# Optimization experiments

Measured on AMD Instinct MI355X. Metric: run time of the kernel, lower is better.

The kernel has to match this reference:

```python
import jax, jax.numpy as jnp
import numpy as np


def _dwconv(x, w, b, pad):
    # x: [B, C, H, W]; w: [C, 1, kh, kw]; depthwise via feature_group_count=C
    y = jax.lax.conv_general_dilated(
        x, w, window_strides=(1, 1), padding=pad,
        dimension_numbers=("NCHW", "OIHW", "NCHW"),
        feature_group_count=x.shape[1])
    return y + b[None, :, None, None]


def setup_inputs() -> dict:
    key = jax.random.key(0)
    ks = jax.random.split(key, 16)
    dim, B, H, W = 128, 32, 64, 64
    def w_init(k, shape):
        fan_in = int(np.prod(shape[1:]))
        return jax.random.normal(k, shape, jnp.float32) * (1.0 / np.sqrt(fan_in))
    return {
        "x": jax.random.normal(ks[0], (B, dim, H, W), jnp.float32),
        "w0": w_init(ks[1], (dim, 1, 5, 5)),   "b0": jax.random.normal(ks[2], (dim,), jnp.float32) * 0.01,
        "w0_1": w_init(ks[3], (dim, 1, 1, 7)), "b0_1": jax.random.normal(ks[4], (dim,), jnp.float32) * 0.01,
        "w0_2": w_init(ks[5], (dim, 1, 7, 1)), "b0_2": jax.random.normal(ks[6], (dim,), jnp.float32) * 0.01,
        "w1_1": w_init(ks[7], (dim, 1, 1, 15)), "b1_1": jax.random.normal(ks[8], (dim,), jnp.float32) * 0.01,
        "w1_2": w_init(ks[9], (dim, 1, 15, 1)), "b1_2": jax.random.normal(ks[10], (dim,), jnp.float32) * 0.01,
        "w2_1": w_init(ks[11], (dim, 1, 1, 31)), "b2_1": jax.random.normal(ks[12], (dim,), jnp.float32) * 0.01,
        "w2_2": w_init(ks[13], (dim, 1, 31, 1)), "b2_2": jax.random.normal(ks[14], (dim,), jnp.float32) * 0.01,
    }


def reference(x, w0, b0, w0_1, b0_1, w0_2, b0_2, w1_1, b1_1, w1_2, b1_2, w2_1, b2_1, w2_2, b2_2):
    attn = _dwconv(x, w0, b0, ((2, 2), (2, 2)))
    attn_0 = _dwconv(attn, w0_1, b0_1, ((0, 0), (3, 3)))
    attn_0 = _dwconv(attn_0, w0_2, b0_2, ((3, 3), (0, 0)))
    attn_1 = _dwconv(attn, w1_1, b1_1, ((0, 0), (7, 7)))
    attn_1 = _dwconv(attn_1, w1_2, b1_2, ((7, 7), (0, 0)))
    attn_2 = _dwconv(attn, w2_1, b2_1, ((0, 0), (15, 15)))
    attn_2 = _dwconv(attn_2, w2_2, b2_2, ((15, 15), (0, 0)))
    return jnp.concatenate((x, attn, attn_0, attn_1, attn_2), axis=1)
```

## Files before the change

kernel.cpp:

```cpp
#include <hip/hip_runtime.h>

#define TPB 256

#define XS_STRIDE 76
#define XS_SIZE   (68 * 76)

#define TS_STRIDE 68
#define TS_SIZE   (64 * 68)

__global__ __launch_bounds__(TPB, 4)
void lka_conv5_kernel(const float* __restrict__ x,
                      const float* __restrict__ w0, const float* __restrict__ b0,
                      float* __restrict__ out) {
    __shared__ __align__(16) float xs[XS_SIZE];
    const int tid = threadIdx.x;
    const int plane = blockIdx.x;
    const int b = plane >> 7;
    const int c = plane & 127;
    const float* xp = x + (size_t)plane * 4096;
    float* outb = out + ((size_t)b * 640 + (size_t)c) * 4096;

    {
        const float4 z4 = make_float4(0.f, 0.f, 0.f, 0.f);
        float4* u4 = (float4*)xs;
#pragma unroll
        for (int k = tid; k < XS_SIZE / 4; k += TPB) u4[k] = z4;
    }
    __syncthreads();
    {
        const float4* x4 = (const float4*)xp;
        float4* o4 = (float4*)outb;
#pragma unroll
        for (int s = 0; s < 4; ++s) {
            const int idx = tid + s * TPB;
            const float4 v = x4[idx];
            o4[idx] = v;
            const int r = idx >> 4;
            const int c0 = (idx & 15) << 2;
            *(float4*)&xs[(r + 2) * XS_STRIDE + c0 + 4] = v;
        }
    }
    __syncthreads();
    {
        const int i = tid >> 2;
        const int j0 = (tid & 3) << 4;
        const float* wp = w0 + c * 25;
        const float bias = b0[c];
        float acc[16];
#pragma unroll
        for (int jj = 0; jj < 16; ++jj) acc[jj] = bias;
#pragma unroll
        for (int a = 0; a < 5; ++a) {
            float raw[24];
#pragma unroll
            for (int k = 0; k < 6; ++k)
                *(float4*)&raw[4 * k] = *(const float4*)&xs[(i + a) * XS_STRIDE + j0 + 4 * k];
#pragma unroll
            for (int bb = 0; bb < 5; ++bb) {
                const float w = wp[a * 5 + bb];
#pragma unroll
                for (int jj = 0; jj < 16; ++jj) acc[jj] += raw[jj + bb + 2] * w;
            }
        }
        float* op = outb + (size_t)128 * 4096 + i * 64 + j0;
#pragma unroll
        for (int q = 0; q < 4; ++q)
            ((float4*)op)[q] = make_float4(acc[4 * q], acc[4 * q + 1],
                                           acc[4 * q + 2], acc[4 * q + 3]);
    }
}

template <int K>
__device__ __forceinline__ void branch_pass(
    const int tid, const int c,
    const float* __restrict__ att,
    const float* __restrict__ wh, const float* __restrict__ bh,
    const float* __restrict__ wv, const float* __restrict__ bv,
    float* __restrict__ op0, float* __restrict__ t) {
    constexpr int T = 2 * K + 1;
    constexpr int KA = K + 1;
    constexpr int NW4 = (KA + 16 + K + 3) / 4;
    constexpr int W = 16 + 2 * K;

    {
        const int i = tid >> 2;
        const int j0 = (tid & 3) << 4;
        const float* arow = att + i * 64;
        float raw[4 * NW4];
#pragma unroll
        for (int q = 0; q < NW4; ++q) {
            const int col0 = j0 - KA + 4 * q;
            const bool ok = (unsigned)col0 < 61u;
            const float4 v = *(const float4*)&arow[ok ? col0 : 0];
            raw[4 * q + 0] = ok ? v.x : 0.f;
            raw[4 * q + 1] = ok ? v.y : 0.f;
            raw[4 * q + 2] = ok ? v.z : 0.f;
            raw[4 * q + 3] = ok ? v.w : 0.f;
        }
        const float* whp = wh + c * T;
        const float bias = bh[c];
        float acc[16];
#pragma unroll
        for (int jj = 0; jj < 16; ++jj) acc[jj] = bias;
#pragma unroll
        for (int d = 0; d < T; ++d) {
            const float w = whp[d];
#pragma unroll
            for (int jj = 0; jj < 16; ++jj) acc[jj] += raw[jj + d + 1] * w;
        }
#pragma unroll
        for (int q = 0; q < 4; ++q)
            *(float4*)&t[i * TS_STRIDE + j0 + 4 * q] =
                make_float4(acc[4 * q], acc[4 * q + 1], acc[4 * q + 2], acc[4 * q + 3]);
    }
    __syncthreads();

    {
        const int j = tid & 63;
        const int i0 = (tid >> 6) << 4;
        float win[W];
#pragma unroll
        for (int dd = 0; dd < W; ++dd) {
            const int r = i0 - K + dd;
            const int rc = min(max(r, 0), 63);
            const float v = t[rc * TS_STRIDE + j];
            win[dd] = (r == rc) ? v : 0.f;
        }
        const float* wvp = wv + c * T;
        const float bias = bv[c];
        float acc[16];
#pragma unroll
        for (int ii = 0; ii < 16; ++ii) acc[ii] = bias;
#pragma unroll
        for (int d = 0; d < T; ++d) {
            const float w = wvp[d];
#pragma unroll
            for (int ii = 0; ii < 16; ++ii) acc[ii] += win[ii + d] * w;
        }
        float* op = op0 + i0 * 64 + j;
#pragma unroll
        for (int ii = 0; ii < 16; ++ii) op[ii * 64] = acc[ii];
    }
}

__global__ __launch_bounds__(TPB, 4)
void lka_branch_kernel(float* out,
                       const float* __restrict__ w01, const float* __restrict__ b01,
                       const float* __restrict__ w02, const float* __restrict__ b02,
                       const float* __restrict__ w11, const float* __restrict__ b11,
                       const float* __restrict__ w12, const float* __restrict__ b12,
                       const float* __restrict__ w21, const float* __restrict__ b21,
                       const float* __restrict__ w22, const float* __restrict__ b22) {
    __shared__ __align__(16) float t[TS_SIZE];
    const int tid = threadIdx.x;
    const int plane = blockIdx.x;
    const int b = plane >> 7;
    const int c = plane & 127;
    const float* att = out + ((size_t)b * 640 + 128 + (size_t)c) * 4096;
    float* op = out + ((size_t)b * 640 + (size_t)(2 + blockIdx.y) * 128 + (size_t)c) * 4096;

    if (blockIdx.y == 0)
        branch_pass<3>(tid, c, att, w01, b01, w02, b02, op, t);
    else if (blockIdx.y == 1)
        branch_pass<7>(tid, c, att, w11, b11, w12, b12, op, t);
    else
        branch_pass<15>(tid, c, att, w21, b21, w22, b22, op, t);
}

extern "C" void kernel_launch(void* const* d_in, const int* in_sizes, int n_in,
                              void* d_out, int out_size, void* d_ws, size_t ws_size,
                              hipStream_t stream) {
    const float* x   = (const float*)d_in[0];
    const float* w0  = (const float*)d_in[1];
    const float* b0  = (const float*)d_in[2];
    const float* w01 = (const float*)d_in[3];
    const float* b01 = (const float*)d_in[4];
    const float* w02 = (const float*)d_in[5];
    const float* b02 = (const float*)d_in[6];
    const float* w11 = (const float*)d_in[7];
    const float* b11 = (const float*)d_in[8];
    const float* w12 = (const float*)d_in[9];
    const float* b12 = (const float*)d_in[10];
    const float* w21 = (const float*)d_in[11];
    const float* b21 = (const float*)d_in[12];
    const float* w22 = (const float*)d_in[13];
    const float* b22 = (const float*)d_in[14];
    float* out = (float*)d_out;

    lka_conv5_kernel<<<dim3(4096), dim3(TPB), 0, stream>>>(x, w0, b0, out);
    lka_branch_kernel<<<dim3(4096, 3), dim3(TPB), 0, stream>>>(
        out, w01, b01, w02, b02, w11, b11, w12, b12, w21, b21, w22, b22);
}
```

Baseline: 450.4 us.

## Fuse 5x5 conv and all three separable branches into one per-plane kernel

Merges the two kernels into one block per (batch, channel) plane. The 5x5 depthwise result stays in LDS and feeds all three horizontal/vertical branch passes, so the attn plane is no longer re-read from global memory three times and one launch disappears. The zero-filled padded LDS tile is replaced by clamped, predicated loads, and __syncthreads is swapped for a raw lgkmcnt wait plus s_barrier. In exchange, each block runs the three branches serially with only 4096 blocks instead of 12288 and uses twice the LDS, which may lower occupancy and parallelism.

```diff
diff --git a/kernel.cpp b/kernel.cpp
--- a/kernel.cpp
+++ b/kernel.cpp
@@ -1,32 +1,110 @@
 #include <hip/hip_runtime.h>
 
 #define TPB 256
-
-#define XS_STRIDE 76
-#define XS_SIZE   (68 * 76)
 
 #define TS_STRIDE 68
 #define TS_SIZE   (64 * 68)
 
+__device__ __forceinline__ void sync_lds() {
+    asm volatile("s_waitcnt lgkmcnt(0)" ::: "memory");
+    __builtin_amdgcn_s_barrier();
+}
+
+template <int K>
+__device__ __forceinline__ void h_pass(const int tid, const int c,
+                                       const float* __restrict__ att,
+                                       const float* __restrict__ wh,
+                                       const float* __restrict__ bh,
+                                       float* __restrict__ t) {
+    constexpr int T = 2 * K + 1;
+    constexpr int KA = K + 1;
+    constexpr int NW4 = (KA + 16 + K + 3) / 4;
+    const int i = tid >> 2;
+    const int j0 = (tid & 3) << 4;
+    const float* wp = wh + c * T;
+    const float bias = bh[c];
+    const float* arow = att + i * TS_STRIDE;
+    float raw[4 * NW4];
+#pragma unroll
+    for (int q = 0; q < NW4; ++q) {
+        const int col0 = j0 - KA + 4 * q;
+        const bool ok = (unsigned)col0 < 61u;
+        const float4 v = *(const float4*)&arow[ok ? col0 : 0];
+        raw[4 * q + 0] = ok ? v.x : 0.f;
+        raw[4 * q + 1] = ok ? v.y : 0.f;
+        raw[4 * q + 2] = ok ? v.z : 0.f;
+        raw[4 * q + 3] = ok ? v.w : 0.f;
+    }
+    float acc[16];
+#pragma unroll
+    for (int jj = 0; jj < 16; ++jj) acc[jj] = bias;
+#pragma unroll
+    for (int d = 0; d < T; ++d) {
+        const float w = wp[d];
+#pragma unroll
+        for (int jj = 0; jj < 16; ++jj) acc[jj] += raw[jj + d + 1] * w;
+    }
+#pragma unroll
+    for (int q = 0; q < 4; ++q)
+        *(float4*)&t[i * TS_STRIDE + j0 + 4 * q] =
+            make_float4(acc[4 * q], acc[4 * q + 1], acc[4 * q + 2], acc[4 * q + 3]);
+}
+
+template <int K>
+__device__ __forceinline__ void v_pass(const int tid, const int c,
+                                       const float* __restrict__ t,
+                                       const float* __restrict__ wv,
+                                       const float* __restrict__ bv,
+                                       float* __restrict__ op0) {
+    constexpr int T = 2 * K + 1;
+    constexpr int W = 16 + 2 * K;
+    const int j = tid & 63;
+    const int i0 = (tid >> 6) << 4;
+    const float* wp = wv + c * T;
+    const float bias = bv[c];
+    float win[W];
+#pragma unroll
+    for (int dd = 0; dd < W; ++dd) {
+        const int r = i0 - K + dd;
+        const int rc = min(max(r, 0), 63);
+        const float v = t[rc * TS_STRIDE + j];
+        win[dd] = (r == rc) ? v : 0.f;
+    }
+    float acc[16];
+#pragma unroll
+    for (int ii = 0; ii < 16; ++ii) acc[ii] = bias;
+#pragma unroll
+    for (int d = 0; d < T; ++d) {
+        const float w = wp[d];
+#pragma unroll
+        for (int ii = 0; ii < 16; ++ii) acc[ii] += win[ii + d] * w;
+    }
+    float* op = op0 + i0 * 64 + j;
+#pragma unroll
+    for (int ii = 0; ii < 16; ++ii) op[ii * 64] = acc[ii];
+}
+
 __global__ __launch_bounds__(TPB, 4)
-void lka_conv5_kernel(const float* __restrict__ x,
-                      const float* __restrict__ w0, const float* __restrict__ b0,
+void lka_fused_kernel(const float* __restrict__ x,
+                      const float* __restrict__ w0,  const float* __restrict__ b0,
+                      const float* __restrict__ w01, const float* __restrict__ b01,
+                      const float* __restrict__ w02, const float* __restrict__ b02,
+                      const float* __restrict__ w11, const float* __restrict__ b11,
+                      const float* __restrict__ w12, const float* __restrict__ b12,
+                      const float* __restrict__ w21, const float* __restrict__ b21,
+                      const float* __restrict__ w22, const float* __restrict__ b22,
                       float* __restrict__ out) {
-    __shared__ __align__(16) float xs[XS_SIZE];
+    __shared__ __align__(16) float bufA[TS_SIZE];
+    __shared__ __align__(16) float bufB[TS_SIZE];
+
     const int tid = threadIdx.x;
     const int plane = blockIdx.x;
     const int b = plane >> 7;
     const int c = plane & 127;
+
     const float* xp = x + (size_t)plane * 4096;
     float* outb = out + ((size_t)b * 640 + (size_t)c) * 4096;
 
-    {
-        const float4 z4 = make_float4(0.f, 0.f, 0.f, 0.f);
-        float4* u4 = (float4*)xs;
-#pragma unroll
-        for (int k = tid; k < XS_SIZE / 4; k += TPB) u4[k] = z4;
-    }
-    __syncthreads();
     {
         const float4* x4 = (const float4*)xp;
         float4* o4 = (float4*)outb;
@@ -37,10 +115,11 @@
             o4[idx] = v;
             const int r = idx >> 4;
             const int c0 = (idx & 15) << 2;
-            *(float4*)&xs[(r + 2) * XS_STRIDE + c0 + 4] = v;
+            *(float4*)&bufA[r * TS_STRIDE + c0] = v;
         }
     }
-    __syncthreads();
+    sync_lds();
+
     {
         const int i = tid >> 2;
         const int j0 = (tid & 3) << 4;
@@ -51,10 +130,22 @@
         for (int jj = 0; jj < 16; ++jj) acc[jj] = bias;
 #pragma unroll
         for (int a = 0; a < 5; ++a) {
+            const int r = i + a - 2;
+            const int rc = min(max(r, 0), 63);
+            const bool okr = (r == rc);
+            const float* xrow = bufA + rc * TS_STRIDE;
             float raw[24];
 #pragma unroll
-            for (int k = 0; k < 6; ++k)
-                *(float4*)&raw[4 * k] = *(const float4*)&xs[(i + a) * XS_STRIDE + j0 + 4 * k];
+            for (int k = 0; k < 6; ++k) {
+                const int col0 = j0 - 4 + 4 * k;
+                const bool okc = (unsigned)col0 < 61u;
+                const bool ok = okr && okc;
+                const float4 v = *(const float4*)&xrow[okc ? col0 : 0];
+                raw[4 * k + 0] = ok ? v.x : 0.f;
+                raw[4 * k + 1] = ok ? v.y : 0.f;
+                raw[4 * k + 2] = ok ? v.z : 0.f;
+                raw[4 * k + 3] = ok ? v.w : 0.f;
+            }
 #pragma unroll
             for (int bb = 0; bb < 5; ++bb) {
                 const float w = wp[a * 5 + bb];
@@ -64,107 +155,28 @@
         }
         float* op = outb + (size_t)128 * 4096 + i * 64 + j0;
 #pragma unroll
-        for (int q = 0; q < 4; ++q)
-            ((float4*)op)[q] = make_float4(acc[4 * q], acc[4 * q + 1],
-                                           acc[4 * q + 2], acc[4 * q + 3]);
-    }
-}
-
-template <int K>
-__device__ __forceinline__ void branch_pass(
-    const int tid, const int c,
-    const float* __restrict__ att,
-    const float* __restrict__ wh, const float* __restrict__ bh,
-    const float* __restrict__ wv, const float* __restrict__ bv,
-    float* __restrict__ op0, float* __restrict__ t) {
-    constexpr int T = 2 * K + 1;
-    constexpr int KA = K + 1;
-    constexpr int NW4 = (KA + 16 + K + 3) / 4;
-    constexpr int W = 16 + 2 * K;
-
-    {
-        const int i = tid >> 2;
-        const int j0 = (tid & 3) << 4;
-        const float* arow = att + i * 64;
-        float raw[4 * NW4];
-#pragma unroll
-        for (int q = 0; q < NW4; ++q) {
-            const int col0 = j0 - KA + 4 * q;
-            const bool ok = (unsigned)col0 < 61u;
-            const float4 v = *(const float4*)&arow[ok ? col0 : 0];
-            raw[4 * q + 0] = ok ? v.x : 0.f;
-            raw[4 * q + 1] = ok ? v.y : 0.f;
-            raw[4 * q + 2] = ok ? v.z : 0.f;
-            raw[4 * q + 3] = ok ? v.w : 0.f;
+        for (int q = 0; q < 4; ++q) {
+            const float4 v = make_float4(acc[4 * q], acc[4 * q + 1],
+                                         acc[4 * q + 2], acc[4 * q + 3]);
+            ((float4*)op)[q] = v;
+            *(float4*)&bufB[i * TS_STRIDE + j0 + 4 * q] = v;
         }
-        const float* whp = wh + c * T;
-        const float bias = bh[c];
-        float acc[16];
-#pragma unroll
-        for (int jj = 0; jj < 16; ++jj) acc[jj] = bias;
-#pragma unroll
-        for (int d = 0; d < T; ++d) {
-            const float w = whp[d];
-#pragma unroll
-            for (int jj = 0; jj < 16; ++jj) acc[jj] += raw[jj + d + 1] * w;
-        }
-#pragma unroll
-        for (int q = 0; q < 4; ++q)
-            *(float4*)&t[i * TS_STRIDE + j0 + 4 * q] =
-                make_float4(acc[4 * q], acc[4 * q + 1], acc[4 * q + 2], acc[4 * q + 3]);
-    }
-    __syncthreads();
-
-    {
-        const int j = tid & 63;
-        const int i0 = (tid >> 6) << 4;
-        float win[W];
-#pragma unroll
-        for (int dd = 0; dd < W; ++dd) {
-            const int r = i0 - K + dd;
-            const int rc = min(max(r, 0), 63);
-            const float v = t[rc * TS_STRIDE + j];
-            win[dd] = (r == rc) ? v : 0.f;
-        }
-        const float* wvp = wv + c * T;
-        const float bias = bv[c];
-        float acc[16];
-#pragma unroll
-        for (int ii = 0; ii < 16; ++ii) acc[ii] = bias;
-#pragma unroll
-        for (int d = 0; d < T; ++d) {
-            const float w = wvp[d];
-#pragma unroll
-            for (int ii = 0; ii < 16; ++ii) acc[ii] += win[ii + d] * w;
-        }
-        float* op = op0 + i0 * 64 + j;
-#pragma unroll
-        for (int ii = 0; ii < 16; ++ii) op[ii * 64] = acc[ii];
-    }
-}
-
-__global__ __launch_bounds__(TPB, 4)
-void lka_branch_kernel(float* out,
-                       const float* __restrict__ w01, const float* __restrict__ b01,
-                       const float* __restrict__ w02, const float* __restrict__ b02,
-                       const float* __restrict__ w11, const float* __restrict__ b11,
-                       const float* __restrict__ w12, const float* __restrict__ b12,
-                       const float* __restrict__ w21, const float* __restrict__ b21,
-                       const float* __restrict__ w22, const float* __restrict__ b22) {
-    __shared__ __align__(16) float t[TS_SIZE];
-    const int tid = threadIdx.x;
-    const int plane = blockIdx.x;
-    const int b = plane >> 7;
-    const int c = plane & 127;
-    const float* att = out + ((size_t)b * 640 + 128 + (size_t)c) * 4096;
-    float* op = out + ((size_t)b * 640 + (size_t)(2 + blockIdx.y) * 128 + (size_t)c) * 4096;
-
-    if (blockIdx.y == 0)
-        branch_pass<3>(tid, c, att, w01, b01, w02, b02, op, t);
-    else if (blockIdx.y == 1)
-        branch_pass<7>(tid, c, att, w11, b11, w12, b12, op, t);
-    else
-        branch_pass<15>(tid, c, att, w21, b21, w22, b22, op, t);
+    }
+    sync_lds();
+
+    h_pass<3>(tid, c, bufB, w01, b01, bufA);
+    sync_lds();
+    v_pass<3>(tid, c, bufA, w02, b02, outb + (size_t)2 * 128 * 4096);
+    sync_lds();
+
+    h_pass<7>(tid, c, bufB, w11, b11, bufA);
+    sync_lds();
+    v_pass<7>(tid, c, bufA, w12, b12, outb + (size_t)3 * 128 * 4096);
+    sync_lds();
+
+    h_pass<15>(tid, c, bufB, w21, b21, bufA);
+    sync_lds();
+    v_pass<15>(tid, c, bufA, w22, b22, outb + (size_t)4 * 128 * 4096);
 }
 
 extern "C" void kernel_launch(void* const* d_in, const int* in_sizes, int n_in,
@@ -187,7 +199,6 @@
     const float* b22 = (const float*)d_in[14];
     float* out = (float*)d_out;
 
-    lka_conv5_kernel<<<dim3(4096), dim3(TPB), 0, stream>>>(x, w0, b0, out);
-    lka_branch_kernel<<<dim3(4096, 3), dim3(TPB), 0, stream>>>(
-        out, w01, b01, w02, b02, w11, b11, w12, b12, w21, b21, w22, b22);
-}
+    lka_fused_kernel<<<dim3(4096), dim3(TPB), 0, stream>>>(
+        x, w0, b0, w01, b01, w02, b02, w11, b11, w12, b12, w21, b21, w22, b22, out);
+}
```

After: 417.3 us. 7.3% less time.
